# Performance work log

Measured on AMD Instinct MI355X. Metric: run time of the kernel, lower is better.

The kernel has to match this reference:

```python
import jax, jax.numpy as jnp
import numpy as np

STATE_DIM = 64
NUM_CHANNELS = 128
BATCH = 8
SEQ_LEN = 4096
DT = 0.01


def hippo_matrix(n):
    # hippo[i,j] = sqrt(2i+1)*sqrt(2j+1) if i>j, (i+1) if i==j, 0 otherwise; A = -hippo
    i = np.arange(n)[:, None]
    j = np.arange(n)[None, :]
    m = np.where(i > j, np.sqrt(2 * i + 1.0) * np.sqrt(2 * j + 1.0), 0.0)
    m = m + np.diag(np.arange(1, n + 1).astype(np.float64))
    return jnp.asarray(-m, dtype=jnp.float32)


def setup_inputs() -> dict:
    key = jax.random.key(0)
    k1, k2, k3 = jax.random.split(key, 3)
    signal = jax.random.normal(k1, (BATCH, NUM_CHANNELS, SEQ_LEN), dtype=jnp.float32)
    B = jax.random.normal(k2, (STATE_DIM, NUM_CHANNELS), dtype=jnp.float32) * 0.1
    C = jax.random.normal(k3, (STATE_DIM, NUM_CHANNELS), dtype=jnp.float32) * 0.1
    A = hippo_matrix(STATE_DIM)
    return {"signal": signal, "B": B, "C": C, "A": A, "dt": DT}


def reference(signal, B, C, A, dt):
    n = A.shape[0]
    eye = jnp.eye(n, dtype=signal.dtype)
    # Bilinear (Tustin) discretization, same as the torch module
    inv = jnp.linalg.inv(eye - dt * 0.5 * A)
    A_bar = inv @ (eye + dt * 0.5 * A)          # [N, N]
    B_bar = dt * (inv @ B)                       # [N, C]

    def step(state, x_t):
        # state: [b, n, c], x_t: [b, c]
        state = jnp.einsum('nm,bmc->bnc', A_bar, state) + B_bar[None] * x_t[:, None, :]
        y = jnp.einsum('nc,bnc->bc', C, state)   # sum over state dim
        return state, y

    x = jnp.moveaxis(signal, -1, 0)              # [L, b, c]
    state0 = jnp.zeros((signal.shape[0], n, signal.shape[1]), dtype=signal.dtype)
    _, ys = jax.lax.scan(step, state0, x)        # ys: [L, b, c]
    return jnp.moveaxis(ys, 0, -1)               # [b, c, L]
```

## Files before the change

### kernel.cpp

```cpp
#include <hip/hip_runtime.h>

#define N 64
#define NC 128
#define NB 8
#define LSEQ 4096
#define QC 128
#define NCHUNK (LSEQ/QC)

#define OFF_ABAR 0
#define OFF_AQ   (OFF_ABAR + N*N)
#define OFF_BBAR (OFF_AQ + N*N)
#define OFF_K    (OFF_BBAR + N*NC)
#define OFF_W    (OFF_K + NC*QC)
#define OFF_U    (OFF_W + QC*NC*N)
#define OFF_FS   (OFF_U + NC*QC*N)
#define OFF_ABT  (OFF_FS)
#define OFF_A2   (OFF_FS + 4096)
#define OFF_A2T  (OFF_FS + 2*4096)
#define OFF_A4   (OFF_FS + 3*4096)
#define OFF_A4T  (OFF_FS + 4*4096)

typedef __attribute__((ext_vector_type(8)))  __bf16 bf16x8;
typedef __attribute__((ext_vector_type(16))) float  f32x16;
typedef __attribute__((ext_vector_type(4)))  unsigned int u32x4;

__device__ __forceinline__ float rdlane(float v, int l) {
    return __int_as_float(__builtin_amdgcn_readlane(__float_as_int(v), l));
}

__device__ __forceinline__ void load_row64(const float* __restrict__ p, float (&ar)[64]) {
    const float4* rp = reinterpret_cast<const float4*>(p);
#pragma unroll
    for (int t = 0; t < 16; ++t) {
        float4 v = rp[t];
        ar[4*t+0] = v.x; ar[4*t+1] = v.y; ar[4*t+2] = v.z; ar[4*t+3] = v.w;
    }
}

__device__ __forceinline__ float matvec64(const float (&ar)[64], float v) {
    float a0 = 0.f, a1 = 0.f, a2 = 0.f, a3 = 0.f;
#pragma unroll
    for (int m = 0; m < 64; m += 4) {
        a0 += ar[m+0] * rdlane(v, m+0);
        a1 += ar[m+1] * rdlane(v, m+1);
        a2 += ar[m+2] * rdlane(v, m+2);
        a3 += ar[m+3] * rdlane(v, m+3);
    }
    return (a0 + a1) + (a2 + a3);
}

__device__ __forceinline__ void f2bf_hl(float x, unsigned short& hi, unsigned short& lo) {
    unsigned u = __float_as_uint(x);
    unsigned r = (u + 0x7fffu + ((u >> 16) & 1u)) >> 16;
    hi = (unsigned short)r;
    float fh = __uint_as_float(r << 16);
    float l  = x - fh;
    unsigned ul = __float_as_uint(l);
    unsigned rl = (ul + 0x7fffu + ((ul >> 16) & 1u)) >> 16;
    lo = (unsigned short)rl;
}

__device__ __forceinline__ bf16x8 ld_frag(const unsigned short* p) {
    u32x4 v = *(const u32x4*)p;
    return __builtin_bit_cast(bf16x8, v);
}

__device__ __forceinline__ bf16x8 pack8(const unsigned short* v) {
    u32x4 u;
    u.x = v[0] | ((unsigned)v[1] << 16);
    u.y = v[2] | ((unsigned)v[3] << 16);
    u.z = v[4] | ((unsigned)v[5] << 16);
    u.w = v[6] | ((unsigned)v[7] << 16);
    return __builtin_bit_cast(bf16x8, u);
}

__global__ __launch_bounds__(256) void prep_cols_kernel(const float* __restrict__ A,
    const float* __restrict__ B, const float* __restrict__ dtp,
    float* __restrict__ ws)
{
    __shared__ float AT[64*65];
    const int tid  = threadIdx.x;
    const int wave = tid >> 6;
    const int l    = tid & 63;
    const float dt = dtp[0];
    const float h  = 0.5f * dt;

    for (int idx = tid; idx < 64*64; idx += 256) {
        int row = idx >> 6, i = idx & 63;
        AT[i*65 + row] = A[idx];
    }
    __syncthreads();

    const float rdv = 1.0f / (1.0f - h * AT[l*65 + l]);
    const int colid = blockIdx.x * 4 + wave;

    float r;
    if (colid < 64) {
        int j = colid;
        r = ((l == j) ? 1.0f : 0.0f) + h * AT[j*65 + l];
    } else {
        int c = colid - 64;
        r = B[l*NC + c];
    }

#pragma unroll
    for (int i = 0; i < 64; ++i) {
        float xi = rdlane(r, i) * rdlane(rdv, i);
        float a  = AT[i*65 + l];
        r = fmaf(h * xi, a, r);
        r = (l == i) ? xi : r;
    }

    if (colid < 64) {
        ws[OFF_ABAR + l*64 + colid] = r;
        ws[OFF_ABT  + colid*64 + l] = r;
    } else {
        ws[OFF_BBAR + l*NC + (colid - 64)] = dt * r;
    }
}

__global__ __launch_bounds__(256) void pow_sq_kernel(const float* __restrict__ src,
    const float* __restrict__ srcT, float* __restrict__ dst, float* __restrict__ dstT)
{
    const int tid = threadIdx.x;
    const int wave = tid >> 6;
    const int l = tid & 63;
    const int j = blockIdx.x * 4 + wave;

    float ar[64];
    load_row64(src + l*64, ar);
    float x = srcT[j*64 + l];
    float y = matvec64(ar, x);
    dst[l*64 + j]  = y;
    dstT[j*64 + l] = y;
}

__global__ __launch_bounds__(256, 1) void chains_kernel(const float* __restrict__ C,
    float* __restrict__ ws)
{
    __shared__ float seed[3][64];
    const int bid = blockIdx.x;
    const int tid = threadIdx.x;
    const int w4  = tid >> 6;
    const int l   = tid & 63;

    if (bid < 128) {
        const int c = bid;
        float a4[64];
        load_row64(ws + OFF_A4 + l*64, a4);
        float cur;
        if (w4 == 0) {
            float ab[64];
            load_row64(ws + OFF_ABAR + l*64, ab);
            float t = ws[OFF_BBAR + l*NC + c];
            cur = t;
            t = matvec64(ab, t); seed[0][l] = t;
            t = matvec64(ab, t); seed[1][l] = t;
            t = matvec64(ab, t); seed[2][l] = t;
        }
        __syncthreads();
        if (w4 > 0) cur = seed[w4 - 1][l];
        int p = w4;
#pragma unroll 1
        for (int it = 0; it < 32; ++it) {
            ws[OFF_W + (p*NC + c)*N + l] = cur;
            if (it < 31) { cur = matvec64(a4, cur); p += 4; }
        }
    } else if (bid < 256) {
        const int c = bid - 128;
        float a4t[64];
        load_row64(ws + OFF_A4T + l*64, a4t);
        float cur;
        if (w4 == 0) {
            float abt[64];
            load_row64(ws + OFF_ABT + l*64, abt);
            float t = C[l*NC + c];
            t = matvec64(abt, t); cur = t;
            t = matvec64(abt, t); seed[0][l] = t;
            t = matvec64(abt, t); seed[1][l] = t;
            t = matvec64(abt, t); seed[2][l] = t;
        }
        __syncthreads();
        if (w4 > 0) cur = seed[w4 - 1][l];
        int q = w4;
#pragma unroll 1
        for (int it = 0; it < 32; ++it) {
            ws[OFF_U + (c*QC + q)*N + l] = cur;
            if (it < 31) { cur = matvec64(a4t, cur); q += 4; }
        }
    } else {
        const int j = (bid - 256)*4 + w4;
        float a4[64];
        load_row64(ws + OFF_A4 + l*64, a4);
        float cur = (l == j) ? 1.0f : 0.0f;
#pragma unroll 1
        for (int it = 0; it < 32; ++it) cur = matvec64(a4, cur);
        ws[OFF_AQ + l*64 + j] = cur;
    }
}

__global__ __launch_bounds__(256) void kdot_kernel(const float* __restrict__ C,
    float* __restrict__ ws)
{
    __shared__ float Wt[64*129];
    __shared__ float Cs[64];
    const int tid = threadIdx.x;
    const int c = blockIdx.x;

    for (int idx = tid; idx < 128*64; idx += 256) {
        int p = idx >> 6, n = idx & 63;
        Wt[n*129 + p] = ws[OFF_W + (p*NC + c)*N + n];
    }
    if (tid < 64) Cs[tid] = C[tid*NC + c];
    __syncthreads();
    if (tid < 128) {
        const int p = tid;
        float acc = 0.0f;
#pragma unroll
        for (int n = 0; n < 64; ++n) acc += Wt[n*129 + p] * Cs[n];
        ws[OFF_K + c*QC + p] = acc;
    }
}

#define FKP 136
__global__ __launch_bounds__(256, 2) void fchunk_mfma_kernel(const float* __restrict__ x,
    float* __restrict__ ws)
{
    __shared__ __align__(16) unsigned short Wh[64*FKP], Wl[64*FKP];
    __shared__ __align__(16) unsigned short Xh[64*FKP], Xl[64*FKP];
    const int tid = threadIdx.x;
    const int c = blockIdx.x;
    const int g = blockIdx.y;

    for (int idx = tid; idx < 128*64; idx += 256) {
        int p = idx >> 6, nn = idx & 63;
        float wv = ws[OFF_W + (p*NC + c)*N + nn];
        unsigned short hi, lo; f2bf_hl(wv, hi, lo);
        int kq = 127 - p;
        Wh[nn*FKP + kq] = hi; Wl[nn*FKP + kq] = lo;
    }
    for (int idx = tid; idx < 64*128; idx += 256) {
        int col = idx >> 7, kk = idx & 127;
        int j = g*8 + (col >> 3), b = col & 7;
        float xv = x[((long)(b*NC + c))*LSEQ + j*QC + kk];
        unsigned short hi, lo; f2bf_hl(xv, hi, lo);
        Xh[col*FKP + kk] = hi; Xl[col*FKP + kk] = lo;
    }
    __syncthreads();

    const int l = tid & 63;
    const int w = tid >> 6;
    const int lane2 = l & 31;
    const int h = l >> 5;
    const int mt = w & 1;
    const int nt = w >> 1;

    f32x16 a0 = {}, a1 = {}, a2 = {};
#pragma unroll
    for (int t = 0; t < 8; ++t) {
        bf16x8 ah = ld_frag(&Wh[(mt*32 + lane2)*FKP + 16*t + 8*h]);
        bf16x8 al = ld_frag(&Wl[(mt*32 + lane2)*FKP + 16*t + 8*h]);
        bf16x8 bh = ld_frag(&Xh[(nt*32 + lane2)*FKP + 16*t + 8*h]);
        bf16x8 bl = ld_frag(&Xl[(nt*32 + lane2)*FKP + 16*t + 8*h]);
        a0 = __builtin_amdgcn_mfma_f32_32x32x16_bf16(ah, bh, a0, 0, 0, 0);
        a1 = __builtin_amdgcn_mfma_f32_32x32x16_bf16(al, bh, a1, 0, 0, 0);
        a2 = __builtin_amdgcn_mfma_f32_32x32x16_bf16(ah, bl, a2, 0, 0, 0);
    }
    f32x16 s = a0 + a1 + a2;
    const int col = g*64 + nt*32 + lane2;
    const int j = col >> 3, b = col & 7;
#pragma unroll
    for (int r = 0; r < 16; ++r) {
        int n = mt*32 + (r & 3) + 8*(r >> 2) + 4*h;
        ws[OFF_FS + ((j*NB + b)*NC + c)*N + n] = s[r];
    }
}

__global__ __launch_bounds__(64) void scan_kernel(float* __restrict__ ws)
{
    const int l = threadIdx.x;
    const int b = blockIdx.x >> 7;
    const int c = blockIdx.x & 127;

    float aq[64];
    load_row64(ws + OFF_AQ + l*64, aq);
    float s = ws[OFF_FS + ((0*NB + b)*NC + c)*N + l];
    for (int j = 1; j <= NCHUNK - 2; ++j) {
        float f = ws[OFF_FS + ((j*NB + b)*NC + c)*N + l];
        float a0 = f, a1 = 0.f, a2 = 0.f, a3 = 0.f;
#pragma unroll
        for (int m = 0; m < 64; m += 4) {
            a0 += aq[m+0] * rdlane(s, m+0);
            a1 += aq[m+1] * rdlane(s, m+1);
            a2 += aq[m+2] * rdlane(s, m+2);
            a3 += aq[m+3] * rdlane(s, m+3);
        }
        s = (a0 + a1) + (a2 + a3);
        ws[OFF_FS + ((j*NB + b)*NC + c)*N + l] = s;
    }
}

#define BKP 200
#define UKP 72
__global__ __launch_bounds__(256, 1) void output_mfma_kernel(const float* __restrict__ x,
    const float* __restrict__ ws, float* __restrict__ out)
{
    __shared__ __align__(16) unsigned short krh[256], krl[256];
    __shared__ __align__(16) unsigned short Uh[128*UKP], Ul[128*UKP];
    __shared__ __align__(16) unsigned short Bh[64*BKP], Bl[64*BKP];
    const int tid = threadIdx.x;
    const int c = blockIdx.x;
    const int g = blockIdx.y;

    {
        int I = tid;
        if (I < 256) {
            float kv = (I < 128) ? ws[OFF_K + c*QC + (127 - I)] : 0.0f;
            unsigned short hi, lo; f2bf_hl(kv, hi, lo);
            krh[I] = hi; krl[I] = lo;
        }
    }
    for (int idx = tid; idx < 128*64; idx += 256) {
        int qq = idx >> 6, nn = idx & 63;
        float uv = ws[OFF_U + (c*QC + qq)*N + nn];
        unsigned short hi, lo; f2bf_hl(uv, hi, lo);
        Uh[qq*UKP + nn] = hi; Ul[qq*UKP + nn] = lo;
    }
    for (int idx = tid; idx < 64*128; idx += 256) {
        int col = idx >> 7, kk = idx & 127;
        int j = g*8 + (col >> 3), b = col & 7;
        float xv = x[((long)(b*NC + c))*LSEQ + j*QC + kk];
        unsigned short hi, lo; f2bf_hl(xv, hi, lo);
        Bh[col*BKP + kk] = hi; Bl[col*BKP + kk] = lo;
    }
    for (int idx = tid; idx < 64*64; idx += 256) {
        int col = idx >> 6, nn = idx & 63;
        int j = g*8 + (col >> 3), b = col & 7;
        float sv = (j > 0) ? ws[OFF_FS + (((j-1)*NB + b)*NC + c)*N + nn] : 0.0f;
        unsigned short hi, lo; f2bf_hl(sv, hi, lo);
        Bh[col*BKP + 128 + nn] = hi; Bl[col*BKP + 128 + nn] = lo;
    }
    __syncthreads();

    const int l = tid & 63;
    const int w = tid >> 6;
    const int lane2 = l & 31;
    const int h = l >> 5;
    const int m = w*32 + lane2;

    f32x16 a0[2] = {{}, {}}, a1[2] = {{}, {}}, a2[2] = {{}, {}};

#pragma unroll
    for (int t = 0; t < 12; ++t) {
        bf16x8 ah, al;
        if (t < 8) {
            int I0 = 127 - m + 16*t + 8*h;
            unsigned short vh[8], vl[8];
#pragma unroll
            for (int e = 0; e < 8; ++e) { vh[e] = krh[I0 + e]; vl[e] = krl[I0 + e]; }
            ah = pack8(vh); al = pack8(vl);
        } else {
            int nbase = 16*t - 128 + 8*h;
            ah = ld_frag(&Uh[m*UKP + nbase]);
            al = ld_frag(&Ul[m*UKP + nbase]);
        }
#pragma unroll
        for (int nt = 0; nt < 2; ++nt) {
            bf16x8 bh = ld_frag(&Bh[(nt*32 + lane2)*BKP + 16*t + 8*h]);
            bf16x8 bl = ld_frag(&Bl[(nt*32 + lane2)*BKP + 16*t + 8*h]);
            a0[nt] = __builtin_amdgcn_mfma_f32_32x32x16_bf16(ah, bh, a0[nt], 0, 0, 0);
            a1[nt] = __builtin_amdgcn_mfma_f32_32x32x16_bf16(al, bh, a1[nt], 0, 0, 0);
            a2[nt] = __builtin_amdgcn_mfma_f32_32x32x16_bf16(ah, bl, a2[nt], 0, 0, 0);
        }
    }

#pragma unroll
    for (int nt = 0; nt < 2; ++nt) {
        f32x16 s = a0[nt] + a1[nt] + a2[nt];
        int col = g*64 + nt*32 + lane2;
        int j = col >> 3, b = col & 7;
        float* op = out + ((long)(b*NC + c))*LSEQ + j*QC;
#pragma unroll
        for (int r = 0; r < 16; ++r) {
            int row = w*32 + (r & 3) + 8*(r >> 2) + 4*h;
            op[row] = s[r];
        }
    }
}

extern "C" void kernel_launch(void* const* d_in, const int* in_sizes, int n_in,
                              void* d_out, int out_size, void* d_ws, size_t ws_size,
                              hipStream_t stream)
{
    const float* signal = (const float*)d_in[0];
    const float* B      = (const float*)d_in[1];
    const float* C      = (const float*)d_in[2];
    const float* A      = (const float*)d_in[3];
    const float* dt     = (const float*)d_in[4];
    float* ws  = (float*)d_ws;
    float* out = (float*)d_out;

    hipLaunchKernelGGL(prep_cols_kernel,  dim3(48),     dim3(256), 0, stream, A, B, dt, ws);
    hipLaunchKernelGGL(pow_sq_kernel,     dim3(16),     dim3(256), 0, stream,
                       ws + OFF_ABAR, ws + OFF_ABT, ws + OFF_A2, ws + OFF_A2T);
    hipLaunchKernelGGL(pow_sq_kernel,     dim3(16),     dim3(256), 0, stream,
                       ws + OFF_A2, ws + OFF_A2T, ws + OFF_A4, ws + OFF_A4T);
    hipLaunchKernelGGL(chains_kernel,     dim3(272),    dim3(256), 0, stream, C, ws);
    hipLaunchKernelGGL(kdot_kernel,       dim3(NC),     dim3(256), 0, stream, C, ws);
    hipLaunchKernelGGL(fchunk_mfma_kernel,dim3(NC, 4),  dim3(256), 0, stream, signal, ws);
    hipLaunchKernelGGL(scan_kernel,       dim3(NB*NC),  dim3(64),  0, stream, ws);
    hipLaunchKernelGGL(output_mfma_kernel,dim3(NC, 4),  dim3(256), 0, stream, signal, ws, out);
}
```

Before: 98.75 us.

## Precompute bf16 hi/lo split operands upstream and fuse kernel-dot into chains

The chains kernel now writes the W and U power chains, and the K filter, directly as pre-split bf16 hi/lo arrays in MFMA-ready layout. K is computed inside chains via a wave reduction, so the separate kdot kernel and one launch go away. The scan kernel emits states already split into bf16. The MFMA kernels then load those operands straight from global memory instead of converting fp32 into LDS on every block. This cuts redundant conversion work and LDS footprint, allowing 2 blocks per CU for the output kernel, at the cost of more global reads issued inside the MFMA loops.

Result: faster. 83.10 us, median of 2 (-15.8%).

```diff
diff --git a/kernel.cpp b/kernel.cpp
--- a/kernel.cpp
+++ b/kernel.cpp
@@ -5,20 +5,27 @@
 #define NB 8
 #define LSEQ 4096
 #define QC 128
-#define NCHUNK (LSEQ/QC)
+#define NCHUNK 32
 
 #define OFF_ABAR 0
-#define OFF_AQ   (OFF_ABAR + N*N)
-#define OFF_BBAR (OFF_AQ + N*N)
-#define OFF_K    (OFF_BBAR + N*NC)
-#define OFF_W    (OFF_K + NC*QC)
-#define OFF_U    (OFF_W + QC*NC*N)
-#define OFF_FS   (OFF_U + NC*QC*N)
-#define OFF_ABT  (OFF_FS)
-#define OFF_A2   (OFF_FS + 4096)
-#define OFF_A2T  (OFF_FS + 2*4096)
-#define OFF_A4   (OFF_FS + 3*4096)
-#define OFF_A4T  (OFF_FS + 4*4096)
+#define OFF_AQ   4096
+#define OFF_BBAR 8192
+#define OFF_ABT  16384
+#define OFF_A2   20480
+#define OFF_A2T  24576
+#define OFF_A4   28672
+#define OFF_A4T  32768
+#define OFF_FS   36864
+#define U16_BASE (OFF_FS + NCHUNK*NB*NC*N)
+
+#define OFF_WH 0
+#define OFF_WL (OFF_WH + NC*N*QC)
+#define OFF_UH (OFF_WL + NC*N*QC)
+#define OFF_UL (OFF_UH + NC*QC*N)
+#define OFF_KH (OFF_UL + NC*QC*N)
+#define OFF_KL (OFF_KH + NC*256)
+#define OFF_SH (OFF_KL + NC*256)
+#define OFF_SL (OFF_SH + NCHUNK*NB*NC*N)
 
 typedef __attribute__((ext_vector_type(8)))  __bf16 bf16x8;
 typedef __attribute__((ext_vector_type(16))) float  f32x16;
@@ -60,6 +67,13 @@
     lo = (unsigned short)rl;
 }
 
+__device__ __forceinline__ unsigned pack_hl2(float x0, float x1, unsigned& lo32) {
+    unsigned short h0, l0, h1, l1;
+    f2bf_hl(x0, h0, l0); f2bf_hl(x1, h1, l1);
+    lo32 = (unsigned)l0 | ((unsigned)l1 << 16);
+    return (unsigned)h0 | ((unsigned)h1 << 16);
+}
+
 __device__ __forceinline__ bf16x8 ld_frag(const unsigned short* p) {
     u32x4 v = *(const u32x4*)p;
     return __builtin_bit_cast(bf16x8, v);
@@ -138,7 +152,10 @@
 __global__ __launch_bounds__(256, 1) void chains_kernel(const float* __restrict__ C,
     float* __restrict__ ws)
 {
+    __shared__ float Wlds[128][65];
+    __shared__ float karr[128];
     __shared__ float seed[3][64];
+    unsigned short* u16b = (unsigned short*)(ws + U16_BASE);
     const int bid = blockIdx.x;
     const int tid = threadIdx.x;
     const int w4  = tid >> 6;
@@ -148,6 +165,7 @@
         const int c = bid;
         float a4[64];
         load_row64(ws + OFF_A4 + l*64, a4);
+        const float Cl = C[l*NC + c];
         float cur;
         if (w4 == 0) {
             float ab[64];
@@ -163,8 +181,31 @@
         int p = w4;
 #pragma unroll 1
         for (int it = 0; it < 32; ++it) {
-            ws[OFF_W + (p*NC + c)*N + l] = cur;
+            Wlds[p][l] = cur;
+            float d = Cl * cur;
+            d += __shfl_xor(d, 32, 64); d += __shfl_xor(d, 16, 64);
+            d += __shfl_xor(d, 8, 64);  d += __shfl_xor(d, 4, 64);
+            d += __shfl_xor(d, 2, 64);  d += __shfl_xor(d, 1, 64);
+            if (l == 0) karr[p] = d;
             if (it < 31) { cur = matvec64(a4, cur); p += 4; }
+        }
+        __syncthreads();
+        for (int idx = tid; idx < 64*64; idx += 256) {
+            int n = idx >> 6, i2 = idx & 63;
+            int kq = i2*2;
+            float w0 = Wlds[127 - kq][n];
+            float w1 = Wlds[126 - kq][n];
+            unsigned lo32, hi32 = pack_hl2(w0, w1, lo32);
+            ((unsigned*)(u16b + OFF_WH + (c*64 + n)*128))[i2] = hi32;
+            ((unsigned*)(u16b + OFF_WL + (c*64 + n)*128))[i2] = lo32;
+        }
+        if (tid < 128) {
+            int i = tid;
+            float k0 = (2*i   < 128) ? karr[127 - 2*i] : 0.0f;
+            float k1 = (2*i+1 < 128) ? karr[126 - 2*i] : 0.0f;
+            unsigned lo32, hi32 = pack_hl2(k0, k1, lo32);
+            ((unsigned*)(u16b + OFF_KH + c*256))[i] = hi32;
+            ((unsigned*)(u16b + OFF_KL + c*256))[i] = lo32;
         }
     } else if (bid < 256) {
         const int c = bid - 128;
@@ -185,7 +226,9 @@
         int q = w4;
 #pragma unroll 1
         for (int it = 0; it < 32; ++it) {
-            ws[OFF_U + (c*QC + q)*N + l] = cur;
+            unsigned short hi, lo; f2bf_hl(cur, hi, lo);
+            u16b[OFF_UH + (c*QC + q)*64 + l] = hi;
+            u16b[OFF_UL + (c*QC + q)*64 + l] = lo;
             if (it < 31) { cur = matvec64(a4t, cur); q += 4; }
         }
     } else {
@@ -199,52 +242,23 @@
     }
 }
 
-__global__ __launch_bounds__(256) void kdot_kernel(const float* __restrict__ C,
-    float* __restrict__ ws)
-{
-    __shared__ float Wt[64*129];
-    __shared__ float Cs[64];
-    const int tid = threadIdx.x;
-    const int c = blockIdx.x;
-
-    for (int idx = tid; idx < 128*64; idx += 256) {
-        int p = idx >> 6, n = idx & 63;
-        Wt[n*129 + p] = ws[OFF_W + (p*NC + c)*N + n];
-    }
-    if (tid < 64) Cs[tid] = C[tid*NC + c];
-    __syncthreads();
-    if (tid < 128) {
-        const int p = tid;
-        float acc = 0.0f;
-#pragma unroll
-        for (int n = 0; n < 64; ++n) acc += Wt[n*129 + p] * Cs[n];
-        ws[OFF_K + c*QC + p] = acc;
-    }
-}
-
-#define FKP 136
 __global__ __launch_bounds__(256, 2) void fchunk_mfma_kernel(const float* __restrict__ x,
     float* __restrict__ ws)
 {
-    __shared__ __align__(16) unsigned short Wh[64*FKP], Wl[64*FKP];
-    __shared__ __align__(16) unsigned short Xh[64*FKP], Xl[64*FKP];
+    __shared__ __align__(16) unsigned Xh32[64*68], Xl32[64*68];
+    const unsigned short* u16b = (const unsigned short*)(ws + U16_BASE);
     const int tid = threadIdx.x;
     const int c = blockIdx.x;
     const int g = blockIdx.y;
 
-    for (int idx = tid; idx < 128*64; idx += 256) {
-        int p = idx >> 6, nn = idx & 63;
-        float wv = ws[OFF_W + (p*NC + c)*N + nn];
-        unsigned short hi, lo; f2bf_hl(wv, hi, lo);
-        int kq = 127 - p;
-        Wh[nn*FKP + kq] = hi; Wl[nn*FKP + kq] = lo;
-    }
-    for (int idx = tid; idx < 64*128; idx += 256) {
-        int col = idx >> 7, kk = idx & 127;
+    for (int idx = tid; idx < 64*64; idx += 256) {
+        int col = idx >> 6, i2 = idx & 63;
         int j = g*8 + (col >> 3), b = col & 7;
-        float xv = x[((long)(b*NC + c))*LSEQ + j*QC + kk];
-        unsigned short hi, lo; f2bf_hl(xv, hi, lo);
-        Xh[col*FKP + kk] = hi; Xl[col*FKP + kk] = lo;
+        const float2 xv = *reinterpret_cast<const float2*>(
+            x + ((long)(b*NC + c))*LSEQ + j*QC + i2*2);
+        unsigned lo32, hi32 = pack_hl2(xv.x, xv.y, lo32);
+        Xh32[col*68 + i2] = hi32;
+        Xl32[col*68 + i2] = lo32;
     }
     __syncthreads();
 
@@ -255,13 +269,18 @@
     const int mt = w & 1;
     const int nt = w >> 1;
 
+    const unsigned short* Xh = (const unsigned short*)Xh32;
+    const unsigned short* Xl = (const unsigned short*)Xl32;
+    const unsigned short* WHp = u16b + OFF_WH + (c*64 + mt*32 + lane2)*128 + 8*h;
+    const unsigned short* WLp = u16b + OFF_WL + (c*64 + mt*32 + lane2)*128 + 8*h;
+
     f32x16 a0 = {}, a1 = {}, a2 = {};
 #pragma unroll
     for (int t = 0; t < 8; ++t) {
-        bf16x8 ah = ld_frag(&Wh[(mt*32 + lane2)*FKP + 16*t + 8*h]);
-        bf16x8 al = ld_frag(&Wl[(mt*32 + lane2)*FKP + 16*t + 8*h]);
-        bf16x8 bh = ld_frag(&Xh[(nt*32 + lane2)*FKP + 16*t + 8*h]);
-        bf16x8 bl = ld_frag(&Xl[(nt*32 + lane2)*FKP + 16*t + 8*h]);
+        bf16x8 ah = ld_frag(WHp + 16*t);
+        bf16x8 al = ld_frag(WLp + 16*t);
+        bf16x8 bh = ld_frag(&Xh[(nt*32 + lane2)*136 + 16*t + 8*h]);
+        bf16x8 bl = ld_frag(&Xl[(nt*32 + lane2)*136 + 16*t + 8*h]);
         a0 = __builtin_amdgcn_mfma_f32_32x32x16_bf16(ah, bh, a0, 0, 0, 0);
         a1 = __builtin_amdgcn_mfma_f32_32x32x16_bf16(al, bh, a1, 0, 0, 0);
         a2 = __builtin_amdgcn_mfma_f32_32x32x16_bf16(ah, bl, a2, 0, 0, 0);
@@ -278,13 +297,23 @@
 
 __global__ __launch_bounds__(64) void scan_kernel(float* __restrict__ ws)
 {
+    unsigned short* u16b = (unsigned short*)(ws + U16_BASE);
     const int l = threadIdx.x;
     const int b = blockIdx.x >> 7;
     const int c = blockIdx.x & 127;
 
     float aq[64];
     load_row64(ws + OFF_AQ + l*64, aq);
+
+    u16b[OFF_SH + ((0*NB + b)*NC + c)*64 + l] = 0;
+    u16b[OFF_SL + ((0*NB + b)*NC + c)*64 + l] = 0;
+
     float s = ws[OFF_FS + ((0*NB + b)*NC + c)*N + l];
+    {
+        unsigned short hi, lo; f2bf_hl(s, hi, lo);
+        u16b[OFF_SH + ((1*NB + b)*NC + c)*64 + l] = hi;
+        u16b[OFF_SL + ((1*NB + b)*NC + c)*64 + l] = lo;
+    }
     for (int j = 1; j <= NCHUNK - 2; ++j) {
         float f = ws[OFF_FS + ((j*NB + b)*NC + c)*N + l];
         float a0 = f, a1 = 0.f, a2 = 0.f, a3 = 0.f;
@@ -296,49 +325,34 @@
             a3 += aq[m+3] * rdlane(s, m+3);
         }
         s = (a0 + a1) + (a2 + a3);
-        ws[OFF_FS + ((j*NB + b)*NC + c)*N + l] = s;
-    }
-}
-
-#define BKP 200
-#define UKP 72
-__global__ __launch_bounds__(256, 1) void output_mfma_kernel(const float* __restrict__ x,
+        unsigned short hi, lo; f2bf_hl(s, hi, lo);
+        u16b[OFF_SH + (((j+1)*NB + b)*NC + c)*64 + l] = hi;
+        u16b[OFF_SL + (((j+1)*NB + b)*NC + c)*64 + l] = lo;
+    }
+}
+
+__global__ __launch_bounds__(256, 2) void output_mfma_kernel(const float* __restrict__ x,
     const float* __restrict__ ws, float* __restrict__ out)
 {
-    __shared__ __align__(16) unsigned short krh[256], krl[256];
-    __shared__ __align__(16) unsigned short Uh[128*UKP], Ul[128*UKP];
-    __shared__ __align__(16) unsigned short Bh[64*BKP], Bl[64*BKP];
+    __shared__ __align__(16) unsigned krh32[128], krl32[128];
+    __shared__ __align__(16) unsigned Xh32[64*68], Xl32[64*68];
+    const unsigned short* u16b = (const unsigned short*)(ws + U16_BASE);
     const int tid = threadIdx.x;
     const int c = blockIdx.x;
     const int g = blockIdx.y;
 
-    {
-        int I = tid;
-        if (I < 256) {
-            float kv = (I < 128) ? ws[OFF_K + c*QC + (127 - I)] : 0.0f;
-            unsigned short hi, lo; f2bf_hl(kv, hi, lo);
-            krh[I] = hi; krl[I] = lo;
-        }
-    }
-    for (int idx = tid; idx < 128*64; idx += 256) {
-        int qq = idx >> 6, nn = idx & 63;
-        float uv = ws[OFF_U + (c*QC + qq)*N + nn];
-        unsigned short hi, lo; f2bf_hl(uv, hi, lo);
-        Uh[qq*UKP + nn] = hi; Ul[qq*UKP + nn] = lo;
-    }
-    for (int idx = tid; idx < 64*128; idx += 256) {
-        int col = idx >> 7, kk = idx & 127;
+    if (tid < 128) {
+        krh32[tid] = ((const unsigned*)(u16b + OFF_KH + c*256))[tid];
+        krl32[tid] = ((const unsigned*)(u16b + OFF_KL + c*256))[tid];
+    }
+    for (int idx = tid; idx < 64*64; idx += 256) {
+        int col = idx >> 6, i2 = idx & 63;
         int j = g*8 + (col >> 3), b = col & 7;
-        float xv = x[((long)(b*NC + c))*LSEQ + j*QC + kk];
-        unsigned short hi, lo; f2bf_hl(xv, hi, lo);
-        Bh[col*BKP + kk] = hi; Bl[col*BKP + kk] = lo;
-    }
-    for (int idx = tid; idx < 64*64; idx += 256) {
-        int col = idx >> 6, nn = idx & 63;
-        int j = g*8 + (col >> 3), b = col & 7;
-        float sv = (j > 0) ? ws[OFF_FS + (((j-1)*NB + b)*NC + c)*N + nn] : 0.0f;
-        unsigned short hi, lo; f2bf_hl(sv, hi, lo);
-        Bh[col*BKP + 128 + nn] = hi; Bl[col*BKP + 128 + nn] = lo;
+        const float2 xv = *reinterpret_cast<const float2*>(
+            x + ((long)(b*NC + c))*LSEQ + j*QC + i2*2);
+        unsigned lo32, hi32 = pack_hl2(xv.x, xv.y, lo32);
+        Xh32[col*68 + i2] = hi32;
+        Xl32[col*68 + i2] = lo32;
     }
     __syncthreads();
 
@@ -348,6 +362,11 @@
     const int h = l >> 5;
     const int m = w*32 + lane2;
 
+    const unsigned short* krh = (const unsigned short*)krh32;
+    const unsigned short* krl = (const unsigned short*)krl32;
+    const unsigned short* Xh = (const unsigned short*)Xh32;
+    const unsigned short* Xl = (const unsigned short*)Xl32;
+
     f32x16 a0[2] = {{}, {}}, a1[2] = {{}, {}}, a2[2] = {{}, {}};
 
 #pragma unroll
@@ -360,14 +379,23 @@
             for (int e = 0; e < 8; ++e) { vh[e] = krh[I0 + e]; vl[e] = krl[I0 + e]; }
             ah = pack8(vh); al = pack8(vl);
         } else {
-            int nbase = 16*t - 128 + 8*h;
-            ah = ld_frag(&Uh[m*UKP + nbase]);
-            al = ld_frag(&Ul[m*UKP + nbase]);
+            const unsigned short* up = u16b + (c*QC + m)*64 + 16*(t-8) + 8*h;
+            ah = ld_frag(up + OFF_UH);
+            al = ld_frag(up + OFF_UL);
         }
 #pragma unroll
         for (int nt = 0; nt < 2; ++nt) {
-            bf16x8 bh = ld_frag(&Bh[(nt*32 + lane2)*BKP + 16*t + 8*h]);
-            bf16x8 bl = ld_frag(&Bl[(nt*32 + lane2)*BKP + 16*t + 8*h]);
+            bf16x8 bh, bl;
+            if (t < 8) {
+                bh = ld_frag(&Xh[(nt*32 + lane2)*136 + 16*t + 8*h]);
+                bl = ld_frag(&Xl[(nt*32 + lane2)*136 + 16*t + 8*h]);
+            } else {
+                int col = g*64 + nt*32 + lane2;
+                int j = col >> 3, b = col & 7;
+                const unsigned short* sp = u16b + ((j*NB + b)*NC + c)*64 + 16*(t-8) + 8*h;
+                bh = ld_frag(sp + OFF_SH);
+                bl = ld_frag(sp + OFF_SL);
+            }
             a0[nt] = __builtin_amdgcn_mfma_f32_32x32x16_bf16(ah, bh, a0[nt], 0, 0, 0);
             a1[nt] = __builtin_amdgcn_mfma_f32_32x32x16_bf16(al, bh, a1[nt], 0, 0, 0);
             a2[nt] = __builtin_amdgcn_mfma_f32_32x32x16_bf16(ah, bl, a2[nt], 0, 0, 0);
@@ -406,7 +434,6 @@
     hipLaunchKernelGGL(pow_sq_kernel,     dim3(16),     dim3(256), 0, stream,
                        ws + OFF_A2, ws + OFF_A2T, ws + OFF_A4, ws + OFF_A4T);
     hipLaunchKernelGGL(chains_kernel,     dim3(272),    dim3(256), 0, stream, C, ws);
-    hipLaunchKernelGGL(kdot_kernel,       dim3(NC),     dim3(256), 0, stream, C, ws);
     hipLaunchKernelGGL(fchunk_mfma_kernel,dim3(NC, 4),  dim3(256), 0, stream, signal, ws);
     hipLaunchKernelGGL(scan_kernel,       dim3(NB*NC),  dim3(64),  0, stream, ws);
     hipLaunchKernelGGL(output_mfma_kernel,dim3(NC, 4),  dim3(256), 0, stream, signal, ws, out);
```
